# Performance work log

Measured on AMD Instinct MI355X. Metric: run time of the kernel, lower is better.

## Reference

```python
import math
import jax, jax.numpy as jnp
import numpy as np

C = 1024  # n_embd
B, T = 4, 2048
H = 4 * C  # mlp hidden
EPS = 1e-5


def setup_inputs() -> dict:
    key = jax.random.key(0)
    ks = jax.random.split(key, 8)
    s = 0.02
    return {
        "x": jax.random.normal(ks[0], (B, T, C), jnp.float32),
        "ln1_g": jnp.ones((C,), jnp.float32),
        "ln1_b": jnp.zeros((C,), jnp.float32),
        "w_attn": jax.random.normal(ks[1], (C, 3 * C), jnp.float32) * s,
        "b_attn": jnp.zeros((3 * C,), jnp.float32),
        "w_proj": jax.random.normal(ks[2], (C, C), jnp.float32) * s,
        "b_proj": jnp.zeros((C,), jnp.float32),
        "ln2_g": jnp.ones((C,), jnp.float32),
        "ln2_b": jnp.zeros((C,), jnp.float32),
        "w_fc": jax.random.normal(ks[3], (C, H), jnp.float32) * s,
        "b_fc": jnp.zeros((H,), jnp.float32),
        "w_mlp_proj": jax.random.normal(ks[4], (H, C), jnp.float32) * s,
        "b_mlp_proj": jnp.zeros((C,), jnp.float32),
    }


def _layernorm(x, g, b):
    mu = jnp.mean(x, axis=-1, keepdims=True)
    var = jnp.mean(jnp.square(x - mu), axis=-1, keepdims=True)
    return (x - mu) * jax.lax.rsqrt(var + EPS) * g + b


def _new_gelu(x):
    c = math.sqrt(2.0 / math.pi)
    return 0.5 * x * (1.0 + jnp.tanh(c * (x + 0.044715 * x * x * x)))


def reference(x, ln1_g, ln1_b, w_attn, b_attn, w_proj, b_proj,
              ln2_g, ln2_b, w_fc, b_fc, w_mlp_proj, b_mlp_proj):
    # --- attention sublayer (single-head, full-dim, no causal mask) ---
    h = _layernorm(x, ln1_g, ln1_b)
    qkv = h @ w_attn + b_attn              # [B,T,3C]
    q, k, v = jnp.split(qkv, 3, axis=-1)   # each [B,T,C]
    scale = 1.0 / math.sqrt(C)
    att = jnp.einsum("btc,bsc->bts", q, k) * scale  # [B,T,T]
    att = jax.nn.softmax(att, axis=-1)
    y = jnp.einsum("bts,bsc->btc", att, v)
    y = y @ w_proj + b_proj
    x = x + y
    # --- MLP sublayer ---
    h2 = _layernorm(x, ln2_g, ln2_b)
    m = _new_gelu(h2 @ w_fc + b_fc) @ w_mlp_proj + b_mlp_proj
    return x + m
```

## Files before the change

kernel.cpp:

```cpp
#include <hip/hip_runtime.h>

typedef __bf16 bf16;
typedef bf16 bf16x8 __attribute__((ext_vector_type(8)));
typedef bf16 bf16x4 __attribute__((ext_vector_type(4)));
typedef float f32x16 __attribute__((ext_vector_type(16)));

#define C_DIM 1024
#define T_DIM 2048
#define B_DIM 4
#define H_DIM 4096

__device__ inline void gld_lds16(const bf16* g, bf16* l) {
    __builtin_amdgcn_global_load_lds(
        (const __attribute__((address_space(1))) unsigned int*)g,
        (__attribute__((address_space(3))) unsigned int*)l,
        16, 0, 0);
}

__device__ inline float fast_gelu(float u) {
    float k2 = 1.5957691216057308f * u + 0.07135480895843475f * u * u * u;
    float t = __expf(-k2);
    return u * __builtin_amdgcn_rcpf(1.0f + t);
}

template <int EPI, typename OutT>
__launch_bounds__(256, 3)
__global__ void gemm_bt(const bf16* __restrict__ A, int lda, long long sA,
                        const bf16* __restrict__ Bt, int ldb, long long sB,
                        OutT* __restrict__ Cout, int ldc, long long sC,
                        const float* __restrict__ bias,
                        const float* __restrict__ resid, long long sR,
                        float alpha, int K) {
    const int z = blockIdx.z;
    A += (long long)z * sA;
    Bt += (long long)z * sB;
    Cout += (long long)z * sC;
    if (resid) resid += (long long)z * sR;

    const int rowBase = blockIdx.x * 128;
    const int colBase = blockIdx.y * 128;

    __shared__ __align__(16) bf16 As[128 * 64];
    __shared__ __align__(16) bf16 Bs[128 * 64];

    const int tid = threadIdx.x;
    const int w = tid >> 6, lane = tid & 63;
    const int wm = w & 1, wn = w >> 1;
    const int ln31 = lane & 31, lh = lane >> 5;

    const int srow = tid >> 3;
    const int scol = ((tid & 7) ^ (srow & 7)) << 3;
    const bf16* Abase = A + (size_t)(rowBase + srow) * lda + scol;
    const bf16* Bbase = Bt + (size_t)(colBase + srow) * ldb + scol;
    bf16* ldsA = As + (size_t)(w * 64) * 8;
    bf16* ldsB = Bs + (size_t)(w * 64) * 8;

    const int rA = wm * 64 + ln31;
    const int rB = wn * 64 + ln31;
    const int swA = rA & 7, swB = rB & 7;

    f32x16 acc[2][2] = {};

    for (int k0 = 0; k0 < K; k0 += 64) {
        __syncthreads();
#pragma unroll
        for (int t = 0; t < 4; t++) {
            gld_lds16(Abase + (size_t)(t * 32) * lda + k0, ldsA + t * 2048);
            gld_lds16(Bbase + (size_t)(t * 32) * ldb + k0, ldsB + t * 2048);
        }
        __syncthreads();
#pragma unroll
        for (int ks = 0; ks < 4; ks++) {
            bf16x8 af[2], bfv[2];
            const int cc = (ks << 1) | lh;
#pragma unroll
            for (int i = 0; i < 2; i++)
                af[i] = *(const bf16x8*)(As + (rA + i * 32) * 64 + ((cc ^ swA) << 3));
#pragma unroll
            for (int j = 0; j < 2; j++)
                bfv[j] = *(const bf16x8*)(Bs + (rB + j * 32) * 64 + ((cc ^ swB) << 3));
#pragma unroll
            for (int i = 0; i < 2; i++)
#pragma unroll
                for (int j = 0; j < 2; j++)
                    acc[i][j] = __builtin_amdgcn_mfma_f32_32x32x16_bf16(af[i], bfv[j], acc[i][j], 0, 0, 0);
        }
    }

    float bval[2];
#pragma unroll
    for (int j = 0; j < 2; j++)
        bval[j] = bias ? bias[colBase + wn * 64 + j * 32 + ln31] : 0.0f;
#pragma unroll
    for (int i = 0; i < 2; i++) {
        const int rtile = rowBase + wm * 64 + i * 32 + 4 * lh;
#pragma unroll
        for (int j = 0; j < 2; j++) {
            const int col = colBase + wn * 64 + j * 32 + ln31;
#pragma unroll
            for (int reg = 0; reg < 16; reg++) {
                const int row = rtile + (reg & 3) + 8 * (reg >> 2);
                float v = acc[i][j][reg] * alpha + bval[j];
                if constexpr (EPI == 1) {
                    v = fast_gelu(v);
                }
                if constexpr (EPI == 2) {
                    v += resid[(size_t)row * ldc + col];
                }
                Cout[(size_t)row * ldc + col] = (OutT)v;
            }
        }
    }
}

__launch_bounds__(256)
__global__ void ln_kernel(const float* __restrict__ x, const float* __restrict__ g,
                          const float* __restrict__ b, bf16* __restrict__ out) {
    __shared__ float red[4];
    const int row = blockIdx.x;
    const int tid = threadIdx.x;
    const float4* xr = (const float4*)(x + (size_t)row * C_DIM);
    float4 v = xr[tid];
    float s = v.x + v.y + v.z + v.w;
#pragma unroll
    for (int m = 32; m; m >>= 1) s += __shfl_xor(s, m, 64);
    if ((tid & 63) == 0) red[tid >> 6] = s;
    __syncthreads();
    const float mu = (red[0] + red[1] + red[2] + red[3]) * (1.0f / C_DIM);
    const float dx = v.x - mu, dy = v.y - mu, dz = v.z - mu, dw = v.w - mu;
    float q = dx * dx + dy * dy + dz * dz + dw * dw;
#pragma unroll
    for (int m = 32; m; m >>= 1) q += __shfl_xor(q, m, 64);
    __syncthreads();
    if ((tid & 63) == 0) red[tid >> 6] = q;
    __syncthreads();
    const float var = (red[0] + red[1] + red[2] + red[3]) * (1.0f / C_DIM);
    const float rs = rsqrtf(var + 1e-5f);
    const float4 gg = ((const float4*)g)[tid];
    const float4 bb = ((const float4*)b)[tid];
    bf16x4 o;
    o[0] = (bf16)(dx * rs * gg.x + bb.x);
    o[1] = (bf16)(dy * rs * gg.y + bb.y);
    o[2] = (bf16)(dz * rs * gg.z + bb.z);
    o[3] = (bf16)(dw * rs * gg.w + bb.w);
    ((bf16x4*)(out + (size_t)row * C_DIM))[tid] = o;
}

__launch_bounds__(256)
__global__ void softmax_kernel(const bf16* __restrict__ S, bf16* __restrict__ P) {
    __shared__ float red[4];
    const size_t base = (size_t)blockIdx.x * T_DIM;
    const int tid = threadIdx.x;
    bf16x8 sv = ((const bf16x8*)(S + base))[tid];
    float e[8];
#pragma unroll
    for (int i = 0; i < 8; i++) e[i] = (float)sv[i];
    float mx = e[0];
#pragma unroll
    for (int i = 1; i < 8; i++) mx = fmaxf(mx, e[i]);
#pragma unroll
    for (int m = 32; m; m >>= 1) mx = fmaxf(mx, __shfl_xor(mx, m, 64));
    if ((tid & 63) == 0) red[tid >> 6] = mx;
    __syncthreads();
    mx = fmaxf(fmaxf(red[0], red[1]), fmaxf(red[2], red[3]));
    float s = 0.0f;
#pragma unroll
    for (int i = 0; i < 8; i++) {
        e[i] = __expf(e[i] - mx);
        s += e[i];
    }
#pragma unroll
    for (int m = 32; m; m >>= 1) s += __shfl_xor(s, m, 64);
    __syncthreads();
    if ((tid & 63) == 0) red[tid >> 6] = s;
    __syncthreads();
    const float inv = 1.0f / (red[0] + red[1] + red[2] + red[3]);
    bf16x8 p;
#pragma unroll
    for (int i = 0; i < 8; i++) p[i] = (bf16)(e[i] * inv);
    ((bf16x8*)(P + base))[tid] = p;
}

__global__ void transpose_f2b_all(const float* __restrict__ s0, bf16* __restrict__ d0,
                                  const float* __restrict__ s1, bf16* __restrict__ d1,
                                  const float* __restrict__ s2, bf16* __restrict__ d2,
                                  const float* __restrict__ s3, bf16* __restrict__ d3) {
    __shared__ float tile[32][33];
    int id = blockIdx.x;
    const float* src;
    bf16* dst;
    int R, Cc, local;
    if (id < 3072)       { src = s0; dst = d0; R = 1024; Cc = 3072; local = id; }
    else if (id < 4096)  { src = s1; dst = d1; R = 1024; Cc = 1024; local = id - 3072; }
    else if (id < 8192)  { src = s2; dst = d2; R = 1024; Cc = 4096; local = id - 4096; }
    else                 { src = s3; dst = d3; R = 4096; Cc = 1024; local = id - 8192; }
    const int tilesX = Cc >> 5;
    const int bx = (local % tilesX) * 32;
    const int by = (local / tilesX) * 32;
    const int tx = threadIdx.x, ty = threadIdx.y;
    for (int i = ty; i < 32; i += 8)
        tile[i][tx] = src[(size_t)(by + i) * Cc + bx + tx];
    __syncthreads();
    for (int i = ty; i < 32; i += 8)
        dst[(size_t)(bx + i) * R + by + tx] = (bf16)tile[tx][i];
}

__global__ void transpose_b2b(const bf16* __restrict__ src, int ldsrc, long long sstride,
                              bf16* __restrict__ dst, long long dstride, int R) {
    __shared__ bf16 tile[32][33];
    src += (long long)blockIdx.z * sstride;
    dst += (long long)blockIdx.z * dstride;
    const int bx = blockIdx.x * 32;
    const int by = blockIdx.y * 32;
    const int tx = threadIdx.x, ty = threadIdx.y;
    for (int i = ty; i < 32; i += 8)
        tile[i][tx] = src[(size_t)(by + i) * ldsrc + bx + tx];
    __syncthreads();
    for (int i = ty; i < 32; i += 8)
        dst[(size_t)(bx + i) * R + by + tx] = tile[tx][i];
}

extern "C" void kernel_launch(void* const* d_in, const int* in_sizes, int n_in,
                              void* d_out, int out_size, void* d_ws, size_t ws_size,
                              hipStream_t stream) {
    const float* x      = (const float*)d_in[0];
    const float* ln1_g  = (const float*)d_in[1];
    const float* ln1_b  = (const float*)d_in[2];
    const float* w_attn = (const float*)d_in[3];
    const float* b_attn = (const float*)d_in[4];
    const float* w_proj = (const float*)d_in[5];
    const float* b_proj = (const float*)d_in[6];
    const float* ln2_g  = (const float*)d_in[7];
    const float* ln2_b  = (const float*)d_in[8];
    const float* w_fc   = (const float*)d_in[9];
    const float* b_fc   = (const float*)d_in[10];
    const float* w_mlp  = (const float*)d_in[11];
    const float* b_mlp  = (const float*)d_in[12];
    float* out = (float*)d_out;

    const int M = B_DIM * T_DIM;

    char* base = (char*)d_ws;
    size_t off = 0;
    auto alloc = [&](size_t bytes) -> char* {
        char* p = base + off;
        off += (bytes + 255) & ~(size_t)255;
        return p;
    };
    bf16* wT_attn = (bf16*)alloc((size_t)3072 * 1024 * 2);
    bf16* wT_proj = (bf16*)alloc((size_t)1024 * 1024 * 2);
    bf16* wT_fc   = (bf16*)alloc((size_t)4096 * 1024 * 2);
    bf16* wT_mlp  = (bf16*)alloc((size_t)1024 * 4096 * 2);
    bf16* h       = (bf16*)alloc((size_t)M * 1024 * 2);
    bf16* qkv     = (bf16*)alloc((size_t)M * 3072 * 2);
    bf16* vT      = (bf16*)alloc((size_t)B_DIM * 1024 * 2048 * 2);
    bf16* S       = (bf16*)alloc((size_t)B_DIM * 2048 * 2048 * 2);
    bf16* P       = (bf16*)alloc((size_t)B_DIM * 2048 * 2048 * 2);
    bf16* y       = (bf16*)alloc((size_t)M * 1024 * 2);
    float* x2     = (float*)alloc((size_t)M * 1024 * 4);
    bf16* act     = (bf16*)S;

    const dim3 tb(32, 8);

    transpose_f2b_all<<<12288, tb, 0, stream>>>(w_attn, wT_attn, w_proj, wT_proj,
                                                w_fc, wT_fc, w_mlp, wT_mlp);

    ln_kernel<<<M, 256, 0, stream>>>(x, ln1_g, ln1_b, h);

    gemm_bt<0, bf16><<<dim3(64, 24, 1), 256, 0, stream>>>(
        h, 1024, 0, wT_attn, 1024, 0, qkv, 3072, 0, b_attn, nullptr, 0, 1.0f, 1024);

    transpose_b2b<<<dim3(1024 / 32, 2048 / 32, B_DIM), tb, 0, stream>>>(
        qkv + 2 * C_DIM, 3072, (long long)T_DIM * 3072, vT, (long long)C_DIM * T_DIM, T_DIM);

    gemm_bt<0, bf16><<<dim3(16, 16, B_DIM), 256, 0, stream>>>(
        qkv, 3072, (long long)T_DIM * 3072,
        qkv + C_DIM, 3072, (long long)T_DIM * 3072,
        S, 2048, (long long)T_DIM * T_DIM, nullptr, nullptr, 0, 0.03125f, 1024);

    softmax_kernel<<<B_DIM * T_DIM, 256, 0, stream>>>(S, P);

    gemm_bt<0, bf16><<<dim3(16, 8, B_DIM), 256, 0, stream>>>(
        P, 2048, (long long)T_DIM * T_DIM,
        vT, 2048, (long long)C_DIM * T_DIM,
        y, 1024, (long long)T_DIM * C_DIM, nullptr, nullptr, 0, 1.0f, 2048);

    gemm_bt<2, float><<<dim3(64, 8, 1), 256, 0, stream>>>(
        y, 1024, 0, wT_proj, 1024, 0, x2, 1024, 0, b_proj, x, 0, 1.0f, 1024);

    ln_kernel<<<M, 256, 0, stream>>>(x2, ln2_g, ln2_b, h);

    gemm_bt<1, bf16><<<dim3(64, 32, 1), 256, 0, stream>>>(
        h, 1024, 0, wT_fc, 1024, 0, act, 4096, 0, b_fc, nullptr, 0, 1.0f, 1024);

    gemm_bt<2, float><<<dim3(64, 8, 1), 256, 0, stream>>>(
        act, 4096, 0, wT_mlp, 4096, 0, out, 1024, 0, b_mlp, x2, 0, 1.0f, 4096);
}
```

Measured before the change: 526.8 us.

## Replace GEMM with 8-wave 256-row tiles and double-buffered async LDS pipeline

Replaces the 128x128 single-buffered GEMM with a 512-thread kernel using 256xBN tiles (BN of 128 or 256 per call site). K-slices are double-buffered in LDS and prefetched with global_load_lds. Partial vmcnt waits and barriers interleave the loads with 16x16x32 MFMA phases, and MFMA issue is raised with s_setprio. The goal is to hide global-load latency and raise arithmetic intensity per block, at the cost of more registers and LDS per block and fewer blocks for the smaller GEMMs.

```diff
diff --git a/kernel.cpp b/kernel.cpp
--- a/kernel.cpp
+++ b/kernel.cpp
@@ -3,7 +3,7 @@
 typedef __bf16 bf16;
 typedef bf16 bf16x8 __attribute__((ext_vector_type(8)));
 typedef bf16 bf16x4 __attribute__((ext_vector_type(4)));
-typedef float f32x16 __attribute__((ext_vector_type(16)));
+typedef float f32x4 __attribute__((ext_vector_type(4)));
 
 #define C_DIM 1024
 #define T_DIM 2048
@@ -23,91 +23,166 @@
     return u * __builtin_amdgcn_rcpf(1.0f + t);
 }
 
-template <int EPI, typename OutT>
-__launch_bounds__(256, 3)
-__global__ void gemm_bt(const bf16* __restrict__ A, int lda, long long sA,
-                        const bf16* __restrict__ Bt, int ldb, long long sB,
-                        OutT* __restrict__ Cout, int ldc, long long sC,
-                        const float* __restrict__ bias,
-                        const float* __restrict__ resid, long long sR,
-                        float alpha, int K) {
+template <int EPI, typename OutT, int BN>
+__launch_bounds__(512, 2)
+__global__ void gemm8p(const bf16* __restrict__ A, int lda, long long sA,
+                       const bf16* __restrict__ Bt, int ldb, long long sB,
+                       OutT* __restrict__ Cout, int ldc, long long sC,
+                       const float* __restrict__ bias,
+                       const float* __restrict__ resid, long long sR,
+                       float alpha, int K) {
+    constexpr int FN = BN / 64;
+    constexpr int BQ = BN / 128;
+
     const int z = blockIdx.z;
     A += (long long)z * sA;
     Bt += (long long)z * sB;
     Cout += (long long)z * sC;
     if (resid) resid += (long long)z * sR;
 
-    const int rowBase = blockIdx.x * 128;
-    const int colBase = blockIdx.y * 128;
-
-    __shared__ __align__(16) bf16 As[128 * 64];
-    __shared__ __align__(16) bf16 Bs[128 * 64];
+    const int rowBase = blockIdx.x * 256;
+    const int colBase = blockIdx.y * BN;
+
+    __shared__ __align__(16) bf16 As[2 * 2 * 256 * 32];
+    __shared__ __align__(16) bf16 Bs[2 * 2 * BN * 32];
 
     const int tid = threadIdx.x;
-    const int w = tid >> 6, lane = tid & 63;
-    const int wm = w & 1, wn = w >> 1;
-    const int ln31 = lane & 31, lh = lane >> 5;
-
-    const int srow = tid >> 3;
-    const int scol = ((tid & 7) ^ (srow & 7)) << 3;
-    const bf16* Abase = A + (size_t)(rowBase + srow) * lda + scol;
-    const bf16* Bbase = Bt + (size_t)(colBase + srow) * ldb + scol;
-    bf16* ldsA = As + (size_t)(w * 64) * 8;
-    bf16* ldsB = Bs + (size_t)(w * 64) * 8;
-
-    const int rA = wm * 64 + ln31;
-    const int rB = wn * 64 + ln31;
-    const int swA = rA & 7, swB = rB & 7;
-
-    f32x16 acc[2][2] = {};
-
-    for (int k0 = 0; k0 < K; k0 += 64) {
-        __syncthreads();
-#pragma unroll
-        for (int t = 0; t < 4; t++) {
-            gld_lds16(Abase + (size_t)(t * 32) * lda + k0, ldsA + t * 2048);
-            gld_lds16(Bbase + (size_t)(t * 32) * ldb + k0, ldsB + t * 2048);
-        }
-        __syncthreads();
-#pragma unroll
-        for (int ks = 0; ks < 4; ks++) {
-            bf16x8 af[2], bfv[2];
-            const int cc = (ks << 1) | lh;
-#pragma unroll
-            for (int i = 0; i < 2; i++)
-                af[i] = *(const bf16x8*)(As + (rA + i * 32) * 64 + ((cc ^ swA) << 3));
-#pragma unroll
-            for (int j = 0; j < 2; j++)
-                bfv[j] = *(const bf16x8*)(Bs + (rB + j * 32) * 64 + ((cc ^ swB) << 3));
-#pragma unroll
-            for (int i = 0; i < 2; i++)
-#pragma unroll
-                for (int j = 0; j < 2; j++)
-                    acc[i][j] = __builtin_amdgcn_mfma_f32_32x32x16_bf16(af[i], bfv[j], acc[i][j], 0, 0, 0);
-        }
+    const int w = tid >> 6;
+    const int lane = tid & 63;
+    const int wm = w >> 2, wn = w & 3;
+    const int lr = lane & 15, lc = lane >> 4;
+
+    const bf16* Ag = A + (size_t)(rowBase + (tid >> 2)) * lda + (tid & 3) * 8;
+    const bf16* Bg = Bt + (size_t)(colBase + (tid >> 2)) * ldb + (tid & 3) * 8;
+    const size_t ldaL = (size_t)lda, ldbL = (size_t)ldb;
+    bf16* AsW = As + w * 512;
+    bf16* BsW = Bs + w * 512;
+
+    const int aBase = wm * 4096 + lr * 32 + lc * 8;
+    const int bBase = wn * (FN * 512) + lr * 32 + lc * 8;
+
+#define STAGE_A(buf, ks, tau) do {                                         \
+        const bf16* _g = Ag + (size_t)(tau) * 64 + (ks) * 32;              \
+        bf16* _l = AsW + ((buf) * 2 + (ks)) * 8192;                        \
+        gld_lds16(_g, _l);                                                 \
+        gld_lds16(_g + 128 * ldaL, _l + 4096);                             \
+    } while (0)
+
+#define STAGE_B(buf, ks, tau) do {                                         \
+        const bf16* _g = Bg + (size_t)(tau) * 64 + (ks) * 32;              \
+        bf16* _l = BsW + ((buf) * 2 + (ks)) * (BN * 32);                   \
+        gld_lds16(_g, _l);                                                 \
+        if constexpr (BQ == 2) gld_lds16(_g + 128 * ldbL, _l + 4096);      \
+    } while (0)
+
+#define LOAD_A(buf, ks, rh) do {                                           \
+        _Pragma("unroll")                                                  \
+        for (int i = 0; i < 4; i++)                                        \
+            af[i] = *(const bf16x8*)(As + aBase + ((buf) * 2 + (ks)) * 8192 \
+                                     + (rh) * 2048 + i * 512);             \
+    } while (0)
+
+#define LOAD_B(dst, buf, ks) do {                                          \
+        _Pragma("unroll")                                                  \
+        for (int j = 0; j < FN; j++)                                       \
+            dst[j] = *(const bf16x8*)(Bs + bBase + ((buf) * 2 + (ks)) * (BN * 32) \
+                                      + j * 512);                          \
+    } while (0)
+
+#define MMA(rh, bfr) do {                                                  \
+        __builtin_amdgcn_s_setprio(1);                                     \
+        _Pragma("unroll")                                                  \
+        for (int i = 0; i < 4; i++)                                        \
+            _Pragma("unroll")                                              \
+            for (int j = 0; j < FN; j++)                                   \
+                acc[(rh) * 4 + i][j] = __builtin_amdgcn_mfma_f32_16x16x32_bf16( \
+                    af[i], bfr[j], acc[(rh) * 4 + i][j], 0, 0, 0);         \
+        __builtin_amdgcn_s_setprio(0);                                     \
+    } while (0)
+
+#define BAR() do { __builtin_amdgcn_s_barrier(); __builtin_amdgcn_sched_barrier(0); } while (0)
+
+#define VMW_STEADY() do {                                                  \
+        if constexpr (BN == 256) asm volatile("s_waitcnt vmcnt(6)" ::: "memory"); \
+        else                     asm volatile("s_waitcnt vmcnt(4)" ::: "memory"); \
+    } while (0)
+#define VMW0() asm volatile("s_waitcnt vmcnt(0)" ::: "memory")
+
+    f32x4 acc[8][FN] = {};
+    bf16x8 af[4], b0[FN], b1[FN];
+
+    const int NT = K >> 6;
+
+    STAGE_B(0, 0, 0);
+    STAGE_A(0, 0, 0);
+    STAGE_B(0, 1, 0);
+    STAGE_A(0, 1, 0);
+    STAGE_B(1, 0, 1);
+    STAGE_A(1, 0, 1);
+    STAGE_B(1, 1, 1);
+    VMW_STEADY();
+    BAR();
+
+    for (int t = 0; t < NT; t += 2) {
+        const bool more2 = (t + 2 < NT);
+
+        LOAD_A(0, 0, 0); LOAD_B(b0, 0, 0);
+        STAGE_A(1, 1, t + 1);
+        BAR(); MMA(0, b0); BAR();
+        LOAD_A(0, 0, 1);
+        if (more2) STAGE_B(0, 0, t + 2);
+        BAR(); MMA(1, b0); BAR();
+        LOAD_A(0, 1, 0); LOAD_B(b1, 0, 1);
+        if (more2) STAGE_A(0, 0, t + 2);
+        BAR(); MMA(0, b1); BAR();
+        LOAD_A(0, 1, 1);
+        if (more2) STAGE_B(0, 1, t + 2);
+        BAR(); MMA(1, b1);
+        if (more2) VMW_STEADY(); else VMW0();
+        BAR();
+
+        LOAD_A(1, 0, 0); LOAD_B(b0, 1, 0);
+        if (more2) STAGE_A(0, 1, t + 2);
+        BAR(); MMA(0, b0); BAR();
+        LOAD_A(1, 0, 1);
+        if (more2) STAGE_B(1, 0, t + 3);
+        BAR(); MMA(1, b0); BAR();
+        LOAD_A(1, 1, 0); LOAD_B(b1, 1, 1);
+        if (more2) STAGE_A(1, 0, t + 3);
+        BAR(); MMA(0, b1); BAR();
+        LOAD_A(1, 1, 1);
+        if (more2) STAGE_B(1, 1, t + 3);
+        BAR(); MMA(1, b1);
+        if (more2) VMW_STEADY();
+        BAR();
     }
 
-    float bval[2];
-#pragma unroll
-    for (int j = 0; j < 2; j++)
-        bval[j] = bias ? bias[colBase + wn * 64 + j * 32 + ln31] : 0.0f;
-#pragma unroll
-    for (int i = 0; i < 2; i++) {
-        const int rtile = rowBase + wm * 64 + i * 32 + 4 * lh;
-#pragma unroll
-        for (int j = 0; j < 2; j++) {
-            const int col = colBase + wn * 64 + j * 32 + ln31;
-#pragma unroll
-            for (int reg = 0; reg < 16; reg++) {
-                const int row = rtile + (reg & 3) + 8 * (reg >> 2);
-                float v = acc[i][j][reg] * alpha + bval[j];
-                if constexpr (EPI == 1) {
-                    v = fast_gelu(v);
-                }
-                if constexpr (EPI == 2) {
-                    v += resid[(size_t)row * ldc + col];
-                }
-                Cout[(size_t)row * ldc + col] = (OutT)v;
+#undef STAGE_A
+#undef STAGE_B
+#undef LOAD_A
+#undef LOAD_B
+#undef MMA
+#undef BAR
+#undef VMW_STEADY
+#undef VMW0
+
+    float bval[FN];
+#pragma unroll
+    for (int j = 0; j < FN; j++)
+        bval[j] = bias ? bias[colBase + wn * (FN * 16) + j * 16 + lr] : 0.0f;
+
+#pragma unroll
+    for (int fi = 0; fi < 8; fi++) {
+        const int row = rowBase + wm * 128 + fi * 16 + lc * 4;
+#pragma unroll
+        for (int fj = 0; fj < FN; fj++) {
+            const int col = colBase + wn * (FN * 16) + fj * 16 + lr;
+#pragma unroll
+            for (int r = 0; r < 4; r++) {
+                float v = acc[fi][fj][r] * alpha + bval[fj];
+                if constexpr (EPI == 1) v = fast_gelu(v);
+                if constexpr (EPI == 2) v += resid[(size_t)(row + r) * ldc + col];
+                Cout[(size_t)(row + r) * ldc + col] = (OutT)v;
             }
         }
     }
@@ -267,32 +342,32 @@
 
     ln_kernel<<<M, 256, 0, stream>>>(x, ln1_g, ln1_b, h);
 
-    gemm_bt<0, bf16><<<dim3(64, 24, 1), 256, 0, stream>>>(
+    gemm8p<0, bf16, 128><<<dim3(32, 24, 1), 512, 0, stream>>>(
         h, 1024, 0, wT_attn, 1024, 0, qkv, 3072, 0, b_attn, nullptr, 0, 1.0f, 1024);
 
     transpose_b2b<<<dim3(1024 / 32, 2048 / 32, B_DIM), tb, 0, stream>>>(
         qkv + 2 * C_DIM, 3072, (long long)T_DIM * 3072, vT, (long long)C_DIM * T_DIM, T_DIM);
 
-    gemm_bt<0, bf16><<<dim3(16, 16, B_DIM), 256, 0, stream>>>(
+    gemm8p<0, bf16, 256><<<dim3(8, 8, B_DIM), 512, 0, stream>>>(
         qkv, 3072, (long long)T_DIM * 3072,
         qkv + C_DIM, 3072, (long long)T_DIM * 3072,
         S, 2048, (long long)T_DIM * T_DIM, nullptr, nullptr, 0, 0.03125f, 1024);
 
     softmax_kernel<<<B_DIM * T_DIM, 256, 0, stream>>>(S, P);
 
-    gemm_bt<0, bf16><<<dim3(16, 8, B_DIM), 256, 0, stream>>>(
+    gemm8p<0, bf16, 128><<<dim3(8, 8, B_DIM), 512, 0, stream>>>(
         P, 2048, (long long)T_DIM * T_DIM,
         vT, 2048, (long long)C_DIM * T_DIM,
         y, 1024, (long long)T_DIM * C_DIM, nullptr, nullptr, 0, 1.0f, 2048);
 
-    gemm_bt<2, float><<<dim3(64, 8, 1), 256, 0, stream>>>(
+    gemm8p<2, float, 128><<<dim3(32, 8, 1), 512, 0, stream>>>(
         y, 1024, 0, wT_proj, 1024, 0, x2, 1024, 0, b_proj, x, 0, 1.0f, 1024);
 
     ln_kernel<<<M, 256, 0, stream>>>(x2, ln2_g, ln2_b, h);
 
-    gemm_bt<1, bf16><<<dim3(64, 32, 1), 256, 0, stream>>>(
+    gemm8p<1, bf16, 256><<<dim3(32, 16, 1), 512, 0, stream>>>(
         h, 1024, 0, wT_fc, 1024, 0, act, 4096, 0, b_fc, nullptr, 0, 1.0f, 1024);
 
-    gemm_bt<2, float><<<dim3(64, 8, 1), 256, 0, stream>>>(
+    gemm8p<2, float, 128><<<dim3(32, 8, 1), 512, 0, stream>>>(
         act, 4096, 0, wT_mlp, 4096, 0, out, 1024, 0, b_mlp, x2, 0, 1.0f, 4096);
 }
```

New measurement: 534.1 us. Within noise of the previous version (+1.4%).
